# Optimization experiments

Measured on AMD Instinct MI355X. Metric: run time of the kernel, lower is better.

## Reference

```python
import jax, jax.numpy as jnp
import numpy as np
from jax import lax

WSIZE = 11
SIGMA = 1.5
PAD = WSIZE // 2  # 5
C1 = 0.01 ** 2
C2 = 0.03 ** 2


def _gauss1d():
    x = np.arange(WSIZE) - WSIZE // 2
    g = np.exp(-(x.astype(np.float64) ** 2) / (2.0 * SIGMA ** 2))
    g = g / g.sum()
    return jnp.asarray(g, dtype=jnp.float32)


def _blur3d(x, g):
    """Replicate-pad by 5 on D/H/W then apply the separable 11x11x11 Gaussian.
    x: [N, 1, D, H, W]. Mathematically identical to the dense conv3d in the
    original (the 3D window is an exact outer product of the 1D Gaussian)."""
    xp = jnp.pad(x, ((0, 0), (0, 0), (PAD, PAD), (PAD, PAD), (PAD, PAD)), mode='edge')
    dn = ('NCDHW', 'OIDHW', 'NCDHW')
    for kshape in ((1, 1, WSIZE, 1, 1), (1, 1, 1, WSIZE, 1), (1, 1, 1, 1, WSIZE)):
        xp = lax.conv_general_dilated(xp, g.reshape(kshape), (1, 1, 1), 'VALID',
                                      dimension_numbers=dn)
    return xp


def _rerange(img):
    img = jnp.where(img.max() > 128.0, img / 255.0, img)
    img = jnp.where(img.min() < -0.5, (img + 1.0) / 2.0, img)
    return img


def setup_inputs() -> dict:
    key = jax.random.key(0)
    k1, k2 = jax.random.split(key)
    N, C, H, W = 4, 16, 512, 512
    pred = jax.random.uniform(k1, (N, C, H, W), dtype=jnp.float32)
    gt = jax.random.uniform(k2, (N, C, H, W), dtype=jnp.float32)
    return {"pred": pred, "gt": gt}


def reference(pred, gt):
    N = pred.shape[0]
    pred = _rerange(pred)
    gt = _rerange(gt)

    # ---- PSNR (range = 1.0, reduce='sum') ----
    mse = jnp.mean((pred - gt) ** 2, axis=(1, 2, 3))           # [N]
    psnr = jnp.sum(10.0 * jnp.log10(1.0 / mse))                # scalar

    # ---- 3D SSIM over [N,1,C,H,W] volumes ----
    g = _gauss1d()
    img = pred[:, None]                                        # [N,1,D,H,W]
    gtt = gt[:, None]
    mu1 = _blur3d(img, g)
    mu2 = _blur3d(gtt, g)
    mu1_sq = mu1 * mu1
    mu2_sq = mu2 * mu2
    mu1_mu2 = mu1 * mu2
    sigma1_sq = _blur3d(img * img, g) - mu1_sq
    sigma2_sq = _blur3d(gtt * gtt, g) - mu2_sq
    sigma12 = _blur3d(img * gtt, g) - mu1_mu2

    v1 = 2.0 * sigma12 + C2
    v2 = sigma1_sq + sigma2_sq + C2
    ssim_map = ((2.0 * mu1_mu2 + C1) * v1) / ((mu1_sq + mu2_sq + C1) * v2)
    ssim = jnp.sum(jnp.mean(ssim_map, axis=(1, 2, 3, 4)))      # reduce='sum'

    return psnr, ssim, N
```

## Files before the change

kernel.cpp:

```cpp
#include <hip/hip_runtime.h>
#include <cmath>


#define NB 4
#define DD 16
#define HH 512
#define WW 512
#define SLICE (HH * WW)
#define VOL (DD * SLICE)
#define C1F 0.0001f
#define C2F 0.0009f

#define TH 16
#define TW 32
#define SH 26
#define SW 42
#define ST4 43
#define NTHR 512
#define NIT 3

struct GW { float g[11]; };

__device__ inline float block_sum512(float v) {
#pragma unroll
  for (int o = 32; o > 0; o >>= 1) v += __shfl_down(v, o, 64);
  __shared__ float r[8];
  if ((threadIdx.x & 63) == 0) r[threadIdx.x >> 6] = v;
  __syncthreads();
  float out = 0.f;
  if (threadIdx.x == 0) {
#pragma unroll
    for (int i = 0; i < 8; ++i) out += r[i];
  }
  __syncthreads();
  return out;
}

__global__ void zero_acc_k(float* acc) {
  if (threadIdx.x < 8) acc[threadIdx.x] = 0.f;
}

__global__ __launch_bounds__(NTHR, 3) void fused_k(
    const float* __restrict__ pred, const float* __restrict__ gt,
    float* __restrict__ acc, GW gw) {
  __shared__ float4 sd4[SH * ST4];
  __shared__ float4 tmp[TH * ST4];
  __shared__ float WL[DD * DD];
  int b = blockIdx.x;
  int tile = b & 511;
  int n = b >> 9;
  int th0 = (tile >> 4) * TH;
  int tw0 = (tile & 15) * TW;
  int t = threadIdx.x;

  if (t < DD * DD) {
    int dout = t >> 4, d = t & 15;
    float w = 0.f;
#pragma unroll
    for (int k = 0; k < 11; ++k) {
      int j = dout + k - 5; j = j < 0 ? 0 : (j > 15 ? 15 : j);
      if (j == d) w += gw.g[k];
    }
    WL[t] = w;
  }

  int goff[NIT], laddr[NIT];
  bool iv[NIT], own[NIT];
#pragma unroll
  for (int it = 0; it < NIT; ++it) {
    int i = t + it * NTHR;
    iv[it] = i < SH * SW;
    int ii = iv[it] ? i : 0;
    int y = ii / SW, x = ii - y * SW;
    int gy = th0 + y - 5; gy = gy < 0 ? 0 : (gy > HH - 1 ? HH - 1 : gy);
    int gx = tw0 + x - 5; gx = gx < 0 ? 0 : (gx > WW - 1 ? WW - 1 : gx);
    goff[it] = gy * WW + gx;
    laddr[it] = y * ST4 + x;
    own[it] = (y >= 5) && (y < 5 + TH) && (x >= 5) && (x < 5 + TW);
  }
  const float* pbase = pred + (size_t)n * VOL;
  const float* qbase = gt + (size_t)n * VOL;

  float pv[NIT], qv[NIT];
#pragma unroll
  for (int it = 0; it < NIT; ++it) {
    pv[it] = iv[it] ? pbase[goff[it]] : 0.f;
    qv[it] = iv[it] ? qbase[goff[it]] : 0.f;
  }

  float psnr = 0.f;
  float accs[DD][4];
#pragma unroll
  for (int j = 0; j < DD; ++j) {
    accs[j][0] = 0.f; accs[j][1] = 0.f; accs[j][2] = 0.f; accs[j][3] = 0.f;
  }
  __syncthreads();

  int wy = t >> 5, wx = t & 31;
#pragma unroll 1
  for (int d = 0; d < DD; ++d) {
#pragma unroll
    for (int it = 0; it < NIT; ++it) {
      if (iv[it]) {
        float S = pv[it] + qv[it], Dm = pv[it] - qv[it];
        sd4[laddr[it]] = make_float4(S, Dm, S * S, Dm * Dm);
        if (own[it]) psnr = fmaf(Dm, Dm, psnr);
      }
    }
    __syncthreads();
    if (d < DD - 1) {
      const float* pd = pbase + (size_t)(d + 1) * SLICE;
      const float* qd = qbase + (size_t)(d + 1) * SLICE;
#pragma unroll
      for (int it = 0; it < NIT; ++it) {
        if (iv[it]) { pv[it] = pd[goff[it]]; qv[it] = qd[goff[it]]; }
      }
    }
    for (int i = t; i < TH * SW; i += NTHR) {
      int r = i / SW, c = i - r * SW;
      float a0 = 0.f, a1 = 0.f, a2 = 0.f, a3 = 0.f;
#pragma unroll
      for (int k = 0; k < 11; ++k) {
        float4 v = sd4[(r + k) * ST4 + c];
        float g = gw.g[k];
        a0 = fmaf(g, v.x, a0);
        a1 = fmaf(g, v.y, a1);
        a2 = fmaf(g, v.z, a2);
        a3 = fmaf(g, v.w, a3);
      }
      tmp[r * ST4 + c] = make_float4(a0, a1, a2, a3);
    }
    __syncthreads();
    float h0 = 0.f, h1 = 0.f, h2 = 0.f, h3 = 0.f;
#pragma unroll
    for (int k = 0; k < 11; ++k) {
      float4 v = tmp[wy * ST4 + wx + k];
      float g = gw.g[k];
      h0 = fmaf(g, v.x, h0);
      h1 = fmaf(g, v.y, h1);
      h2 = fmaf(g, v.z, h2);
      h3 = fmaf(g, v.w, h3);
    }
    const float* wl = WL + d;
#pragma unroll
    for (int dout = 0; dout < DD; ++dout) {
      float w = wl[dout * DD];
      accs[dout][0] = fmaf(w, h0, accs[dout][0]);
      accs[dout][1] = fmaf(w, h1, accs[dout][1]);
      accs[dout][2] = fmaf(w, h2, accs[dout][2]);
      accs[dout][3] = fmaf(w, h3, accs[dout][3]);
    }
    __syncthreads();
  }

  float ssum = 0.f;
#pragma unroll
  for (int j = 0; j < DD; ++j) {
    float Sb = accs[j][0], Db = accs[j][1], B1 = accs[j][2], B2 = accs[j][3];
    float SS = Sb * Sb, DDm = Db * Db;
    float m12_2 = (SS - DDm) * 0.5f;
    float msq   = (SS + DDm) * 0.5f;
    float Epq   = (B1 - B2) * 0.25f;
    float Esum  = (B1 + B2) * 0.5f;
    float sig12_2 = 2.f * Epq - m12_2;
    float svar    = Esum - msq;
    float num = (m12_2 + C1F) * (sig12_2 + C2F);
    float den = (msq + C1F) * (svar + C2F);
    ssum += num / den;
  }
  float bs = block_sum512(ssum);
  if (t == 0) atomicAdd(&acc[4 + n], bs);
  float bp = block_sum512(psnr);
  if (t == 0) atomicAdd(&acc[n], bp);
}

__global__ void final_k(const float* __restrict__ acc, float* __restrict__ out) {
  if (threadIdx.x == 0 && blockIdx.x == 0) {
    double psnr = 0.0, ssim = 0.0;
    for (int n = 0; n < NB; ++n) {
      double mse = (double)acc[n] / (double)VOL;
      psnr += 10.0 * log10(1.0 / mse);
      ssim += (double)acc[4 + n] / (double)VOL;
    }
    out[0] = (float)psnr;
    out[1] = (float)ssim;
    out[2] = (float)NB;
  }
}

extern "C" void kernel_launch(void* const* d_in, const int* in_sizes, int n_in,
                              void* d_out, int out_size, void* d_ws, size_t ws_size,
                              hipStream_t stream) {
  const float* pred = (const float*)d_in[0];
  const float* gt = (const float*)d_in[1];
  float* acc = (float*)d_ws;
  GW gw;
  double tt[11], s = 0.0;
  for (int i = 0; i < 11; ++i) {
    double x = i - 5;
    tt[i] = exp(-(x * x) / 4.5);
    s += tt[i];
  }
  for (int i = 0; i < 11; ++i) gw.g[i] = (float)(tt[i] / s);

  zero_acc_k<<<1, 64, 0, stream>>>(acc);
  fused_k<<<NB * 512, NTHR, 0, stream>>>(pred, gt, acc, gw);
  final_k<<<1, 1, 0, stream>>>(acc, (float*)d_out);
}
```

Measured before the change: 286.2 us.

## Store blur intermediates as bf16 in LDS, shrink tiles, register-block vertical pass

```diff
diff --git a/kernel.cpp b/kernel.cpp
--- a/kernel.cpp
+++ b/kernel.cpp
@@ -1,4 +1,5 @@
 #include <hip/hip_runtime.h>
+#include <hip/hip_bf16.h>
 #include <cmath>
 
 
@@ -12,26 +13,36 @@
 #define C2F 0.0009f
 
 #define TH 16
-#define TW 32
+#define TW 16
 #define SH 26
-#define SW 42
-#define ST4 43
-#define NTHR 512
+#define SW 26
+#define ST 27
+#define NTHR 256
 #define NIT 3
 
 struct GW { float g[11]; };
 
-__device__ inline float block_sum512(float v) {
+__device__ inline float blo(unsigned v) {
+  union { unsigned u; float f; } c; c.u = v << 16; return c.f;
+}
+__device__ inline float bhi(unsigned v) {
+  union { unsigned u; float f; } c; c.u = v & 0xFFFF0000u; return c.f;
+}
+__device__ inline unsigned pack_bf2(float a, float b) {
+  __hip_bfloat162 t;
+  t.x = __float2bfloat16(a);
+  t.y = __float2bfloat16(b);
+  union { __hip_bfloat162 h; unsigned u; } c; c.h = t; return c.u;
+}
+
+__device__ inline float block_sum256(float v) {
 #pragma unroll
   for (int o = 32; o > 0; o >>= 1) v += __shfl_down(v, o, 64);
-  __shared__ float r[8];
+  __shared__ float r[4];
   if ((threadIdx.x & 63) == 0) r[threadIdx.x >> 6] = v;
   __syncthreads();
   float out = 0.f;
-  if (threadIdx.x == 0) {
-#pragma unroll
-    for (int i = 0; i < 8; ++i) out += r[i];
-  }
+  if (threadIdx.x == 0) out = r[0] + r[1] + r[2] + r[3];
   __syncthreads();
   return out;
 }
@@ -40,17 +51,17 @@
   if (threadIdx.x < 8) acc[threadIdx.x] = 0.f;
 }
 
-__global__ __launch_bounds__(NTHR, 3) void fused_k(
+__global__ __launch_bounds__(NTHR, 4) void fused_k(
     const float* __restrict__ pred, const float* __restrict__ gt,
     float* __restrict__ acc, GW gw) {
-  __shared__ float4 sd4[SH * ST4];
-  __shared__ float4 tmp[TH * ST4];
+  __shared__ uint2 sd[SH * ST];
+  __shared__ uint2 tmp[TH * ST];
   __shared__ float WL[DD * DD];
   int b = blockIdx.x;
-  int tile = b & 511;
-  int n = b >> 9;
-  int th0 = (tile >> 4) * TH;
-  int tw0 = (tile & 15) * TW;
+  int tile = b & 1023;
+  int n = b >> 10;
+  int th0 = (tile >> 5) * TH;
+  int tw0 = (tile & 31) * TW;
   int t = threadIdx.x;
 
   if (t < DD * DD) {
@@ -75,7 +86,7 @@
     int gy = th0 + y - 5; gy = gy < 0 ? 0 : (gy > HH - 1 ? HH - 1 : gy);
     int gx = tw0 + x - 5; gx = gx < 0 ? 0 : (gx > WW - 1 ? WW - 1 : gx);
     goff[it] = gy * WW + gx;
-    laddr[it] = y * ST4 + x;
+    laddr[it] = y * ST + x;
     own[it] = (y >= 5) && (y < 5 + TH) && (x >= 5) && (x < 5 + TW);
   }
   const float* pbase = pred + (size_t)n * VOL;
@@ -89,21 +100,19 @@
   }
 
   float psnr = 0.f;
-  float accs[DD][4];
-#pragma unroll
-  for (int j = 0; j < DD; ++j) {
-    accs[j][0] = 0.f; accs[j][1] = 0.f; accs[j][2] = 0.f; accs[j][3] = 0.f;
-  }
+  float a0[DD], a1[DD], a2[DD], a3[DD];
+#pragma unroll
+  for (int j = 0; j < DD; ++j) { a0[j] = a1[j] = a2[j] = a3[j] = 0.f; }
   __syncthreads();
 
-  int wy = t >> 5, wx = t & 31;
+  int wy = t >> 4, wx = t & 15;
 #pragma unroll 1
   for (int d = 0; d < DD; ++d) {
 #pragma unroll
     for (int it = 0; it < NIT; ++it) {
       if (iv[it]) {
         float S = pv[it] + qv[it], Dm = pv[it] - qv[it];
-        sd4[laddr[it]] = make_float4(S, Dm, S * S, Dm * Dm);
+        sd[laddr[it]] = make_uint2(pack_bf2(S, Dm), pack_bf2(S * S, Dm * Dm));
         if (own[it]) psnr = fmaf(Dm, Dm, psnr);
       }
     }
@@ -116,39 +125,51 @@
         if (iv[it]) { pv[it] = pd[goff[it]]; qv[it] = qd[goff[it]]; }
       }
     }
-    for (int i = t; i < TH * SW; i += NTHR) {
-      int r = i / SW, c = i - r * SW;
-      float a0 = 0.f, a1 = 0.f, a2 = 0.f, a3 = 0.f;
-#pragma unroll
-      for (int k = 0; k < 11; ++k) {
-        float4 v = sd4[(r + k) * ST4 + c];
-        float g = gw.g[k];
-        a0 = fmaf(g, v.x, a0);
-        a1 = fmaf(g, v.y, a1);
-        a2 = fmaf(g, v.z, a2);
-        a3 = fmaf(g, v.w, a3);
+    if (t < 4 * SW) {
+      int strip = t / SW, c = t - strip * SW;
+      int r0 = strip * 4;
+      float h0[4], h1[4], h2[4], h3[4];
+#pragma unroll
+      for (int j = 0; j < 4; ++j) { h0[j] = h1[j] = h2[j] = h3[j] = 0.f; }
+#pragma unroll
+      for (int k = 0; k < 14; ++k) {
+        uint2 v = sd[(r0 + k) * ST + c];
+        float Sv = blo(v.x), Dv = bhi(v.x), S2v = blo(v.y), D2v = bhi(v.y);
+#pragma unroll
+        for (int j = 0; j < 4; ++j) {
+          if (k - j >= 0 && k - j <= 10) {
+            float g = gw.g[k - j];
+            h0[j] = fmaf(g, Sv, h0[j]);
+            h1[j] = fmaf(g, Dv, h1[j]);
+            h2[j] = fmaf(g, S2v, h2[j]);
+            h3[j] = fmaf(g, D2v, h3[j]);
+          }
+        }
       }
-      tmp[r * ST4 + c] = make_float4(a0, a1, a2, a3);
+#pragma unroll
+      for (int j = 0; j < 4; ++j)
+        tmp[(r0 + j) * ST + c] =
+            make_uint2(pack_bf2(h0[j], h1[j]), pack_bf2(h2[j], h3[j]));
     }
     __syncthreads();
-    float h0 = 0.f, h1 = 0.f, h2 = 0.f, h3 = 0.f;
+    float w0 = 0.f, w1 = 0.f, w2 = 0.f, w3 = 0.f;
 #pragma unroll
     for (int k = 0; k < 11; ++k) {
-      float4 v = tmp[wy * ST4 + wx + k];
+      uint2 v = tmp[wy * ST + wx + k];
       float g = gw.g[k];
-      h0 = fmaf(g, v.x, h0);
-      h1 = fmaf(g, v.y, h1);
-      h2 = fmaf(g, v.z, h2);
-      h3 = fmaf(g, v.w, h3);
+      w0 = fmaf(g, blo(v.x), w0);
+      w1 = fmaf(g, bhi(v.x), w1);
+      w2 = fmaf(g, blo(v.y), w2);
+      w3 = fmaf(g, bhi(v.y), w3);
     }
     const float* wl = WL + d;
 #pragma unroll
     for (int dout = 0; dout < DD; ++dout) {
       float w = wl[dout * DD];
-      accs[dout][0] = fmaf(w, h0, accs[dout][0]);
-      accs[dout][1] = fmaf(w, h1, accs[dout][1]);
-      accs[dout][2] = fmaf(w, h2, accs[dout][2]);
-      accs[dout][3] = fmaf(w, h3, accs[dout][3]);
+      a0[dout] = fmaf(w, w0, a0[dout]);
+      a1[dout] = fmaf(w, w1, a1[dout]);
+      a2[dout] = fmaf(w, w2, a2[dout]);
+      a3[dout] = fmaf(w, w3, a3[dout]);
     }
     __syncthreads();
   }
@@ -156,7 +177,7 @@
   float ssum = 0.f;
 #pragma unroll
   for (int j = 0; j < DD; ++j) {
-    float Sb = accs[j][0], Db = accs[j][1], B1 = accs[j][2], B2 = accs[j][3];
+    float Sb = a0[j], Db = a1[j], B1 = a2[j], B2 = a3[j];
     float SS = Sb * Sb, DDm = Db * Db;
     float m12_2 = (SS - DDm) * 0.5f;
     float msq   = (SS + DDm) * 0.5f;
@@ -168,9 +189,9 @@
     float den = (msq + C1F) * (svar + C2F);
     ssum += num / den;
   }
-  float bs = block_sum512(ssum);
+  float bs = block_sum256(ssum);
   if (t == 0) atomicAdd(&acc[4 + n], bs);
-  float bp = block_sum512(psnr);
+  float bp = block_sum256(psnr);
   if (t == 0) atomicAdd(&acc[n], bp);
 }
 
@@ -204,6 +225,6 @@
   for (int i = 0; i < 11; ++i) gw.g[i] = (float)(tt[i] / s);
 
   zero_acc_k<<<1, 64, 0, stream>>>(acc);
-  fused_k<<<NB * 512, NTHR, 0, stream>>>(pred, gt, acc, gw);
+  fused_k<<<NB * 1024, NTHR, 0, stream>>>(pred, gt, acc, gw);
   final_k<<<1, 1, 0, stream>>>(acc, (float*)d_out);
 }
```

Measured after the change: 384.0 us. 1.34x slower.

## Store blur intermediates as packed bf16 in LDS and double-buffer the input slice

Applied to the files above, without the earlier changes.

```diff
diff --git a/kernel.cpp b/kernel.cpp
--- a/kernel.cpp
+++ b/kernel.cpp
@@ -1,4 +1,5 @@
 #include <hip/hip_runtime.h>
+#include <hip/hip_bf16.h>
 #include <cmath>
 
 
@@ -15,11 +16,24 @@
 #define TW 32
 #define SH 26
 #define SW 42
-#define ST4 43
+#define ST 43
 #define NTHR 512
 #define NIT 3
 
 struct GW { float g[11]; };
+
+__device__ inline float blo(unsigned v) {
+  union { unsigned u; float f; } c; c.u = v << 16; return c.f;
+}
+__device__ inline float bhi(unsigned v) {
+  union { unsigned u; float f; } c; c.u = v & 0xFFFF0000u; return c.f;
+}
+__device__ inline unsigned pack_bf2(float a, float b) {
+  __hip_bfloat162 t;
+  t.x = __float2bfloat16(a);
+  t.y = __float2bfloat16(b);
+  union { __hip_bfloat162 h; unsigned u; } c; c.h = t; return c.u;
+}
 
 __device__ inline float block_sum512(float v) {
 #pragma unroll
@@ -40,11 +54,11 @@
   if (threadIdx.x < 8) acc[threadIdx.x] = 0.f;
 }
 
-__global__ __launch_bounds__(NTHR, 3) void fused_k(
+__global__ __launch_bounds__(NTHR, 2) void fused_k(
     const float* __restrict__ pred, const float* __restrict__ gt,
     float* __restrict__ acc, GW gw) {
-  __shared__ float4 sd4[SH * ST4];
-  __shared__ float4 tmp[TH * ST4];
+  __shared__ uint2 sd[2][SH * ST];
+  __shared__ uint2 tmp[TH * ST];
   __shared__ float WL[DD * DD];
   int b = blockIdx.x;
   int tile = b & 511;
@@ -75,7 +89,7 @@
     int gy = th0 + y - 5; gy = gy < 0 ? 0 : (gy > HH - 1 ? HH - 1 : gy);
     int gx = tw0 + x - 5; gx = gx < 0 ? 0 : (gx > WW - 1 ? WW - 1 : gx);
     goff[it] = gy * WW + gx;
-    laddr[it] = y * ST4 + x;
+    laddr[it] = y * ST + x;
     own[it] = (y >= 5) && (y < 5 + TH) && (x >= 5) && (x < 5 + TW);
   }
   const float* pbase = pred + (size_t)n * VOL;
@@ -89,21 +103,20 @@
   }
 
   float psnr = 0.f;
-  float accs[DD][4];
-#pragma unroll
-  for (int j = 0; j < DD; ++j) {
-    accs[j][0] = 0.f; accs[j][1] = 0.f; accs[j][2] = 0.f; accs[j][3] = 0.f;
-  }
+  float a0[DD], a1[DD], a2[DD], a3[DD];
+#pragma unroll
+  for (int j = 0; j < DD; ++j) { a0[j] = a1[j] = a2[j] = a3[j] = 0.f; }
   __syncthreads();
 
   int wy = t >> 5, wx = t & 31;
 #pragma unroll 1
   for (int d = 0; d < DD; ++d) {
+    uint2* sdb = sd[d & 1];
 #pragma unroll
     for (int it = 0; it < NIT; ++it) {
       if (iv[it]) {
         float S = pv[it] + qv[it], Dm = pv[it] - qv[it];
-        sd4[laddr[it]] = make_float4(S, Dm, S * S, Dm * Dm);
+        sdb[laddr[it]] = make_uint2(pack_bf2(S, Dm), pack_bf2(S * S, Dm * Dm));
         if (own[it]) psnr = fmaf(Dm, Dm, psnr);
       }
     }
@@ -118,45 +131,44 @@
     }
     for (int i = t; i < TH * SW; i += NTHR) {
       int r = i / SW, c = i - r * SW;
-      float a0 = 0.f, a1 = 0.f, a2 = 0.f, a3 = 0.f;
+      float h0 = 0.f, h1 = 0.f, h2 = 0.f, h3 = 0.f;
 #pragma unroll
       for (int k = 0; k < 11; ++k) {
-        float4 v = sd4[(r + k) * ST4 + c];
+        uint2 v = sdb[(r + k) * ST + c];
         float g = gw.g[k];
-        a0 = fmaf(g, v.x, a0);
-        a1 = fmaf(g, v.y, a1);
-        a2 = fmaf(g, v.z, a2);
-        a3 = fmaf(g, v.w, a3);
+        h0 = fmaf(g, blo(v.x), h0);
+        h1 = fmaf(g, bhi(v.x), h1);
+        h2 = fmaf(g, blo(v.y), h2);
+        h3 = fmaf(g, bhi(v.y), h3);
       }
-      tmp[r * ST4 + c] = make_float4(a0, a1, a2, a3);
+      tmp[r * ST + c] = make_uint2(pack_bf2(h0, h1), pack_bf2(h2, h3));
     }
     __syncthreads();
-    float h0 = 0.f, h1 = 0.f, h2 = 0.f, h3 = 0.f;
+    float w0 = 0.f, w1 = 0.f, w2 = 0.f, w3 = 0.f;
 #pragma unroll
     for (int k = 0; k < 11; ++k) {
-      float4 v = tmp[wy * ST4 + wx + k];
+      uint2 v = tmp[wy * ST + wx + k];
       float g = gw.g[k];
-      h0 = fmaf(g, v.x, h0);
-      h1 = fmaf(g, v.y, h1);
-      h2 = fmaf(g, v.z, h2);
-      h3 = fmaf(g, v.w, h3);
+      w0 = fmaf(g, blo(v.x), w0);
+      w1 = fmaf(g, bhi(v.x), w1);
+      w2 = fmaf(g, blo(v.y), w2);
+      w3 = fmaf(g, bhi(v.y), w3);
     }
     const float* wl = WL + d;
 #pragma unroll
     for (int dout = 0; dout < DD; ++dout) {
       float w = wl[dout * DD];
-      accs[dout][0] = fmaf(w, h0, accs[dout][0]);
-      accs[dout][1] = fmaf(w, h1, accs[dout][1]);
-      accs[dout][2] = fmaf(w, h2, accs[dout][2]);
-      accs[dout][3] = fmaf(w, h3, accs[dout][3]);
-    }
-    __syncthreads();
+      a0[dout] = fmaf(w, w0, a0[dout]);
+      a1[dout] = fmaf(w, w1, a1[dout]);
+      a2[dout] = fmaf(w, w2, a2[dout]);
+      a3[dout] = fmaf(w, w3, a3[dout]);
+    }
   }
 
   float ssum = 0.f;
 #pragma unroll
   for (int j = 0; j < DD; ++j) {
-    float Sb = accs[j][0], Db = accs[j][1], B1 = accs[j][2], B2 = accs[j][3];
+    float Sb = a0[j], Db = a1[j], B1 = a2[j], B2 = a3[j];
     float SS = Sb * Sb, DDm = Db * Db;
     float m12_2 = (SS - DDm) * 0.5f;
     float msq   = (SS + DDm) * 0.5f;
```

Result: faster. 271.9 us (-5.0%).
